# Kernel optimization log

Hardware: AMD Instinct MI355X
Metric: run time of the kernel (lower is better)

## Reference

```python
import jax, jax.numpy as jnp
import numpy as np

DIM = 1024
HEADS = 16
HEAD_DIM = DIM // HEADS
B, N = 2, 2048


def setup_inputs() -> dict:
    key = jax.random.key(0)
    k1, k2, k3, k4 = jax.random.split(key, 4)
    x = jax.random.normal(k1, (B, N, DIM), dtype=jnp.float32)
    # torch Linear weights: shape (out_features, in_features), y = x @ W.T + b
    w_qkv = jax.random.normal(k2, (3 * DIM, DIM), dtype=jnp.float32) * (DIM ** -0.5)
    w_proj = jax.random.normal(k3, (DIM, DIM), dtype=jnp.float32) * (DIM ** -0.5)
    b_proj = jax.random.normal(k4, (DIM,), dtype=jnp.float32) * 0.01
    return {"x": x, "w_qkv": w_qkv, "w_proj": w_proj, "b_proj": b_proj}


def reference(x, w_qkv, w_proj, b_proj):
    Bb, Nn, D = x.shape
    scale = HEAD_DIM ** -0.5
    qkv = x @ w_qkv.T                                # [B, N, 3D]
    qkv = qkv.reshape(Bb, Nn, 3, HEADS, HEAD_DIM)
    qkv = jnp.transpose(qkv, (2, 0, 3, 1, 4))        # [3, B, H, N, hd]
    q, k, v = qkv[0], qkv[1], qkv[2]
    attn = jnp.einsum('bhqd,bhkd->bhqk', q, k) * scale
    attn = jax.nn.softmax(attn, axis=-1)
    out = jnp.einsum('bhqk,bhkd->bhqd', attn, v)     # [B, H, N, hd]
    out = jnp.transpose(out, (0, 2, 1, 3)).reshape(Bb, Nn, D)
    return out @ w_proj.T + b_proj
```

## Files before the change

kernel.cpp:

```cpp
#include <hip/hip_runtime.h>
#include <cstdint>
#include <cstddef>

using u16 = unsigned short;
using u32 = uint32_t;
using f32x4  = __attribute__((ext_vector_type(4))) float;
using bf16x8 = __attribute__((ext_vector_type(8))) __bf16;
using s16x4  = __attribute__((ext_vector_type(4))) short;

#define D_MODEL 1024
#define N_HEADS 16
#define HD      64
#define SEQ     2048
#define QKV_LD  3072
#define K2SCALE 0.18033688011112042f

__device__ __forceinline__ u16 f2b(float f) {
  union { float f; u32 u; } v; v.f = f;
  u32 r = 0x7FFFu + ((v.u >> 16) & 1u);
  return (u16)((v.u + r) >> 16);
}

__device__ __forceinline__ u32 pkbf16(float a, float b) {
  return (u32)f2b(a) | ((u32)f2b(b) << 16);
}

#define MFMA16(A, B, C) __builtin_amdgcn_mfma_f32_16x16x16bf16_1k(A, B, C, 0, 0, 0)

__device__ __forceinline__ void gld16(const u16* g, u16* l) {
  __builtin_amdgcn_global_load_lds(
      (const __attribute__((address_space(1))) void*)g,
      (__attribute__((address_space(3))) void*)l, 16, 0, 0);
}

__global__ void cast_bf16(const float* __restrict__ src, u16* __restrict__ dst) {
  int i = blockIdx.x * blockDim.x + threadIdx.x;
  float4 f = ((const float4*)src)[i];
  ushort4 o;
  o.x = f2b(f.x); o.y = f2b(f.y); o.z = f2b(f.z); o.w = f2b(f.w);
  ((ushort4*)dst)[i] = o;
}

template<int OUTMODE>
__launch_bounds__(256, 2)
__global__ void gemm_nt(const u16* __restrict__ A, const u16* __restrict__ B,
                        u16* __restrict__ Ob, float* __restrict__ Of,
                        const float* __restrict__ bias, int N, int K) {
  __shared__ __attribute__((aligned(16))) u16 sA[128 * 32];
  __shared__ __attribute__((aligned(16))) u16 sB[128 * 32];

  const int tid  = threadIdx.x;
  const int lane = tid & 63;
  const int w    = tid >> 6;
  const int qd   = lane >> 4;
  const int ln   = lane & 15;
  const int wm   = (w >> 1) * 64;
  const int wn   = (w & 1) * 64;
  const int m0   = blockIdx.y * 128;
  const int n0   = blockIdx.x * 128;

  f32x4 acc[4][4] = {};

  for (int k0 = 0; k0 < K; k0 += 32) {
    __syncthreads();
    #pragma unroll
    for (int c = 0; c < 2; ++c) {
      int sbase = w * 128 + c * 64;
      int s = sbase + lane;
      int row = s >> 2, col = (s & 3) * 8;
      gld16(A + (size_t)(m0 + row) * K + k0 + col, &sA[sbase * 8]);
      gld16(B + (size_t)(n0 + row) * K + k0 + col, &sB[sbase * 8]);
    }
    __syncthreads();

    bf16x8 af[4], bfm[4];
    #pragma unroll
    for (int i = 0; i < 4; ++i) {
      af[i]  = *(const bf16x8*)&sA[(wm + i * 16 + ln) * 32 + qd * 8];
      bfm[i] = *(const bf16x8*)&sB[(wn + i * 16 + ln) * 32 + qd * 8];
    }
    #pragma unroll
    for (int i = 0; i < 4; ++i)
      #pragma unroll
      for (int j = 0; j < 4; ++j)
        acc[i][j] = __builtin_amdgcn_mfma_f32_16x16x32_bf16(af[i], bfm[j], acc[i][j], 0, 0, 0);
  }

  #pragma unroll
  for (int i = 0; i < 4; ++i) {
    #pragma unroll
    for (int j = 0; j < 4; ++j) {
      #pragma unroll
      for (int r = 0; r < 4; ++r) {
        int row = m0 + wm + i * 16 + qd * 4 + r;
        int col = n0 + wn + j * 16 + ln;
        float v = acc[i][j][r];
        if (OUTMODE == 0) {
          if (col < D_MODEL) v *= K2SCALE;
          Ob[(size_t)row * N + col] = f2b(v);
        } else {
          Of[(size_t)row * N + col] = v + bias[col];
        }
      }
    }
  }
}

__launch_bounds__(256, 4)
__global__ void attn_kernel(const u16* __restrict__ qkv, u16* __restrict__ outb) {
  __shared__ __attribute__((aligned(16))) u16 sK[2][128 * 32];
  __shared__ __attribute__((aligned(16))) u32 sVT[64 * 68];

  const int tid  = threadIdx.x;
  const int lane = tid & 63;
  const int w    = tid >> 6;
  const int qd   = lane >> 4;
  const int ln   = lane & 15;
  const int qt   = blockIdx.x;
  const int h    = blockIdx.y & 15;
  const int b    = blockIdx.y >> 4;
  const size_t tokbase = (size_t)b * SEQ;
  const int q0   = qt * 64;
  const int qoff = h * HD;
  const int koff = D_MODEL + h * HD;
  const int voff = 2 * D_MODEL + h * HD;

  bf16x8 aq[2];
  #pragma unroll
  for (int hf = 0; hf < 2; ++hf)
    aq[hf] = *(const bf16x8*)(qkv + (tokbase + q0 + w * 16 + ln) * QKV_LD
                              + qoff + hf * 32 + qd * 8);

  f32x4 accOT[4] = {};
  float psum = 0.0f;

  for (int kt = 0; kt < 16; ++kt) {
    const int kt0 = kt * 128;
    __syncthreads();
    #pragma unroll
    for (int hf = 0; hf < 2; ++hf) {
      #pragma unroll
      for (int c = 0; c < 2; ++c) {
        int sbase = w * 128 + c * 64;
        int s = sbase + lane;
        int row = s >> 2, col = (s & 3) * 8;
        gld16(qkv + (tokbase + kt0 + row) * QKV_LD + koff + hf * 32 + col,
              &sK[hf][sbase * 8]);
      }
    }
    #pragma unroll
    for (int it = 0; it < 2; ++it) {
      int j  = it * 256 + tid;
      int tp = j & 63;
      int d0 = (j >> 6) * 8;
      const u16* g0 = qkv + (tokbase + kt0 + tp * 2) * QKV_LD + voff + d0;
      union { uint4 q; u32 d[4]; } va, vb;
      va.q = *(const uint4*)g0;
      vb.q = *(const uint4*)(g0 + QKV_LD);
      #pragma unroll
      for (int e = 0; e < 4; ++e) {
        sVT[(d0 + 2 * e    ) * 68 + tp] = __builtin_amdgcn_perm(vb.d[e], va.d[e], 0x05040100u);
        sVT[(d0 + 2 * e + 1) * 68 + tp] = __builtin_amdgcn_perm(vb.d[e], va.d[e], 0x07060302u);
      }
    }
    __syncthreads();

    f32x4 accST[8] = {};
    #pragma unroll
    for (int cb = 0; cb < 8; ++cb) {
      #pragma unroll
      for (int hf = 0; hf < 2; ++hf) {
        bf16x8 ak = *(const bf16x8*)&sK[hf][(cb * 16 + ln) * 32 + qd * 8];
        accST[cb] = __builtin_amdgcn_mfma_f32_16x16x32_bf16(ak, aq[hf], accST[cb], 0, 0, 0);
      }
    }

    s16x4 pf[8];
    #pragma unroll
    for (int cb = 0; cb < 8; ++cb) {
      float p0 = __builtin_amdgcn_exp2f(accST[cb][0]);
      float p1 = __builtin_amdgcn_exp2f(accST[cb][1]);
      float p2 = __builtin_amdgcn_exp2f(accST[cb][2]);
      float p3 = __builtin_amdgcn_exp2f(accST[cb][3]);
      psum += (p0 + p1) + (p2 + p3);
      union { u32 d[2]; s16x4 v; } pk;
      pk.d[0] = pkbf16(p0, p1);
      pk.d[1] = pkbf16(p2, p3);
      pf[cb] = pk.v;
    }

    #pragma unroll
    for (int cb = 0; cb < 8; ++cb) {
      #pragma unroll
      for (int ob = 0; ob < 4; ++ob) {
        s16x4 vf = *(const s16x4*)&sVT[(ob * 16 + ln) * 68 + cb * 8 + qd * 2];
        accOT[ob] = MFMA16(vf, pf[cb], accOT[ob]);
      }
    }
  }

  psum += __shfl_xor(psum, 16, 64);
  psum += __shfl_xor(psum, 32, 64);
  const float rinv = 1.0f / psum;

  u16* sOut = (u16*)&sK[0][0];
  __syncthreads();
  #pragma unroll
  for (int ob = 0; ob < 4; ++ob) {
    u32 lo = pkbf16(accOT[ob][0] * rinv, accOT[ob][1] * rinv);
    u32 hi = pkbf16(accOT[ob][2] * rinv, accOT[ob][3] * rinv);
    ((u32*)sOut)[(w * 16 + ln) * 36 + ob * 8 + qd * 2    ] = lo;
    ((u32*)sOut)[(w * 16 + ln) * 36 + ob * 8 + qd * 2 + 1] = hi;
  }
  __syncthreads();
  #pragma unroll
  for (int it = 0; it < 2; ++it) {
    int idx = it * 256 + tid;
    int token = idx >> 3, chunk = idx & 7;
    uint4 v = *(const uint4*)&sOut[token * 72 + chunk * 8];
    *(uint4*)&outb[(tokbase + q0 + token) * D_MODEL + h * HD + chunk * 8] = v;
  }
}

extern "C" void kernel_launch(void* const* d_in, const int* in_sizes, int n_in,
                              void* d_out, int out_size, void* d_ws, size_t ws_size,
                              hipStream_t stream) {
  const float* x      = (const float*)d_in[0];
  const float* w_qkv  = (const float*)d_in[1];
  const float* w_proj = (const float*)d_in[2];
  const float* b_proj = (const float*)d_in[3];
  float* out = (float*)d_out;

  u16* ws     = (u16*)d_ws;
  u16* xb     = ws;
  u16* wqkvb  = xb    + (size_t)4096 * 1024;
  u16* wprojb = wqkvb + (size_t)3072 * 1024;
  u16* qkvb   = wprojb + (size_t)1024 * 1024;
  u16* attnb  = qkvb  + (size_t)4096 * 3072;

  cast_bf16<<<4096, 256, 0, stream>>>(x,      xb);
  cast_bf16<<<3072, 256, 0, stream>>>(w_qkv,  wqkvb);
  cast_bf16<<<1024, 256, 0, stream>>>(w_proj, wprojb);

  gemm_nt<0><<<dim3(24, 32), 256, 0, stream>>>(xb, wqkvb, qkvb, nullptr, nullptr, 3072, 1024);

  attn_kernel<<<dim3(32, 32), 256, 0, stream>>>(qkvb, attnb);

  gemm_nt<1><<<dim3(8, 32), 256, 0, stream>>>(attnb, wprojb, nullptr, out, b_proj, 1024, 1024);
}
```

Measured before the change: 224.1 us.

## Double-buffer attention K/V tiles, process 128 queries per block, shrink proj GEMM tile

The attention kernel now double-buffers K and transposed V in shared memory. It prefetches the next tile's V into registers one iteration ahead and handles two 64-query groups per block, so each K/V tile is reused twice and load latency overlaps compute. Scores are computed and consumed per 16-key chunk instead of being kept for the full 128-key tile. The GEMM gains an M-tile template parameter, and the output projection uses 64-row tiles to launch more blocks, with launch bounds changed to 3 waves per SIMD. In exchange, shared memory and registers per block rise, attention occupancy drops to 2 blocks, and the attention grid halves to 512 blocks.

```diff
diff --git a/kernel.cpp b/kernel.cpp
--- a/kernel.cpp
+++ b/kernel.cpp
@@ -41,12 +41,12 @@
   ((ushort4*)dst)[i] = o;
 }
 
-template<int OUTMODE>
-__launch_bounds__(256, 2)
+template<int OUTMODE, int MT>
+__launch_bounds__(256, 3)
 __global__ void gemm_nt(const u16* __restrict__ A, const u16* __restrict__ B,
                         u16* __restrict__ Ob, float* __restrict__ Of,
                         const float* __restrict__ bias, int N, int K) {
-  __shared__ __attribute__((aligned(16))) u16 sA[128 * 32];
+  __shared__ __attribute__((aligned(16))) u16 sA[MT * 32];
   __shared__ __attribute__((aligned(16))) u16 sB[128 * 32];
 
   const int tid  = threadIdx.x;
@@ -54,40 +54,48 @@
   const int w    = tid >> 6;
   const int qd   = lane >> 4;
   const int ln   = lane & 15;
-  const int wm   = (w >> 1) * 64;
+  constexpr int MI = MT / 32;
+  const int wm   = (w >> 1) * (MT / 2);
   const int wn   = (w & 1) * 64;
-  const int m0   = blockIdx.y * 128;
+  const int m0   = blockIdx.y * MT;
   const int n0   = blockIdx.x * 128;
 
-  f32x4 acc[4][4] = {};
+  f32x4 acc[MI][4] = {};
 
   for (int k0 = 0; k0 < K; k0 += 32) {
     __syncthreads();
+    #pragma unroll
+    for (int c = 0; c < MT / 64; ++c) {
+      int sbase = w * MT + c * 64;
+      int s = sbase + lane;
+      int row = s >> 2, col = (s & 3) * 8;
+      gld16(A + (size_t)(m0 + row) * K + k0 + col, &sA[sbase * 8]);
+    }
     #pragma unroll
     for (int c = 0; c < 2; ++c) {
       int sbase = w * 128 + c * 64;
       int s = sbase + lane;
       int row = s >> 2, col = (s & 3) * 8;
-      gld16(A + (size_t)(m0 + row) * K + k0 + col, &sA[sbase * 8]);
       gld16(B + (size_t)(n0 + row) * K + k0 + col, &sB[sbase * 8]);
     }
     __syncthreads();
 
-    bf16x8 af[4], bfm[4];
-    #pragma unroll
-    for (int i = 0; i < 4; ++i) {
-      af[i]  = *(const bf16x8*)&sA[(wm + i * 16 + ln) * 32 + qd * 8];
-      bfm[i] = *(const bf16x8*)&sB[(wn + i * 16 + ln) * 32 + qd * 8];
-    }
-    #pragma unroll
-    for (int i = 0; i < 4; ++i)
+    bf16x8 af[MI], bfm[4];
+    #pragma unroll
+    for (int i = 0; i < MI; ++i)
+      af[i] = *(const bf16x8*)&sA[(wm + i * 16 + ln) * 32 + qd * 8];
+    #pragma unroll
+    for (int j = 0; j < 4; ++j)
+      bfm[j] = *(const bf16x8*)&sB[(wn + j * 16 + ln) * 32 + qd * 8];
+    #pragma unroll
+    for (int i = 0; i < MI; ++i)
       #pragma unroll
       for (int j = 0; j < 4; ++j)
         acc[i][j] = __builtin_amdgcn_mfma_f32_16x16x32_bf16(af[i], bfm[j], acc[i][j], 0, 0, 0);
   }
 
   #pragma unroll
-  for (int i = 0; i < 4; ++i) {
+  for (int i = 0; i < MI; ++i) {
     #pragma unroll
     for (int j = 0; j < 4; ++j) {
       #pragma unroll
@@ -106,115 +114,140 @@
   }
 }
 
-__launch_bounds__(256, 4)
+__launch_bounds__(256, 2)
 __global__ void attn_kernel(const u16* __restrict__ qkv, u16* __restrict__ outb) {
-  __shared__ __attribute__((aligned(16))) u16 sK[2][128 * 32];
-  __shared__ __attribute__((aligned(16))) u32 sVT[64 * 68];
+  __shared__ __attribute__((aligned(16))) u16 sK[2][2][128 * 32];
+  __shared__ __attribute__((aligned(16))) u32 sVT[2][64 * 68];
 
   const int tid  = threadIdx.x;
   const int lane = tid & 63;
   const int w    = tid >> 6;
   const int qd   = lane >> 4;
   const int ln   = lane & 15;
-  const int qt   = blockIdx.x;
+  const int qp   = blockIdx.x;
   const int h    = blockIdx.y & 15;
   const int b    = blockIdx.y >> 4;
   const size_t tokbase = (size_t)b * SEQ;
-  const int q0   = qt * 64;
+  const int q0   = qp * 128;
   const int qoff = h * HD;
   const int koff = D_MODEL + h * HD;
   const int voff = 2 * D_MODEL + h * HD;
 
-  bf16x8 aq[2];
-  #pragma unroll
-  for (int hf = 0; hf < 2; ++hf)
-    aq[hf] = *(const bf16x8*)(qkv + (tokbase + q0 + w * 16 + ln) * QKV_LD
-                              + qoff + hf * 32 + qd * 8);
-
-  f32x4 accOT[4] = {};
-  float psum = 0.0f;
-
-  for (int kt = 0; kt < 16; ++kt) {
-    const int kt0 = kt * 128;
-    __syncthreads();
-    #pragma unroll
-    for (int hf = 0; hf < 2; ++hf) {
+  bf16x8 aq[2][2];
+  #pragma unroll
+  for (int c2 = 0; c2 < 2; ++c2)
+    #pragma unroll
+    for (int hf = 0; hf < 2; ++hf)
+      aq[c2][hf] = *(const bf16x8*)(qkv + (tokbase + q0 + c2 * 64 + w * 16 + ln) * QKV_LD
+                                    + qoff + hf * 32 + qd * 8);
+
+  auto stageK = [&](int kt, int buf) {
+    #pragma unroll
+    for (int hf = 0; hf < 2; ++hf)
       #pragma unroll
       for (int c = 0; c < 2; ++c) {
         int sbase = w * 128 + c * 64;
         int s = sbase + lane;
         int row = s >> 2, col = (s & 3) * 8;
-        gld16(qkv + (tokbase + kt0 + row) * QKV_LD + koff + hf * 32 + col,
-              &sK[hf][sbase * 8]);
-      }
-    }
+        gld16(qkv + (tokbase + kt * 128 + row) * QKV_LD + koff + hf * 32 + col,
+              &sK[buf][hf][sbase * 8]);
+      }
+  };
+  auto loadV = [&](int kt, uint4* va, uint4* vb) {
     #pragma unroll
     for (int it = 0; it < 2; ++it) {
-      int j  = it * 256 + tid;
-      int tp = j & 63;
-      int d0 = (j >> 6) * 8;
-      const u16* g0 = qkv + (tokbase + kt0 + tp * 2) * QKV_LD + voff + d0;
-      union { uint4 q; u32 d[4]; } va, vb;
-      va.q = *(const uint4*)g0;
-      vb.q = *(const uint4*)(g0 + QKV_LD);
+      int j = it * 256 + tid;
+      int tp = j & 63, d0 = (j >> 6) * 8;
+      const u16* g0 = qkv + (tokbase + kt * 128 + tp * 2) * QKV_LD + voff + d0;
+      va[it] = *(const uint4*)g0;
+      vb[it] = *(const uint4*)(g0 + QKV_LD);
+    }
+  };
+  auto writeV = [&](int buf, const uint4* va, const uint4* vb) {
+    #pragma unroll
+    for (int it = 0; it < 2; ++it) {
+      int j = it * 256 + tid;
+      int tp = j & 63, d0 = (j >> 6) * 8;
+      const u32* a  = (const u32*)&va[it];
+      const u32* bb = (const u32*)&vb[it];
       #pragma unroll
       for (int e = 0; e < 4; ++e) {
-        sVT[(d0 + 2 * e    ) * 68 + tp] = __builtin_amdgcn_perm(vb.d[e], va.d[e], 0x05040100u);
-        sVT[(d0 + 2 * e + 1) * 68 + tp] = __builtin_amdgcn_perm(vb.d[e], va.d[e], 0x07060302u);
-      }
-    }
+        sVT[buf][(d0 + 2 * e    ) * 68 + tp] = __builtin_amdgcn_perm(bb[e], a[e], 0x05040100u);
+        sVT[buf][(d0 + 2 * e + 1) * 68 + tp] = __builtin_amdgcn_perm(bb[e], a[e], 0x07060302u);
+      }
+    }
+  };
+
+  stageK(0, 0);
+  uint4 va[2], vb[2];
+  loadV(0, va, vb);
+  writeV(0, va, vb);
+  loadV(1, va, vb);
+
+  f32x4 accOT[2][4] = {};
+  float psum[2] = {0.f, 0.f};
+
+  for (int kt = 0; kt < 16; ++kt) {
+    const int cur = kt & 1, nxt = cur ^ 1;
     __syncthreads();
-
-    f32x4 accST[8] = {};
+    if (kt < 15) { stageK(kt + 1, nxt); writeV(nxt, va, vb); }
+    if (kt < 14) { loadV(kt + 2, va, vb); }
+
     #pragma unroll
     for (int cb = 0; cb < 8; ++cb) {
-      #pragma unroll
-      for (int hf = 0; hf < 2; ++hf) {
-        bf16x8 ak = *(const bf16x8*)&sK[hf][(cb * 16 + ln) * 32 + qd * 8];
-        accST[cb] = __builtin_amdgcn_mfma_f32_16x16x32_bf16(ak, aq[hf], accST[cb], 0, 0, 0);
-      }
-    }
-
-    s16x4 pf[8];
-    #pragma unroll
-    for (int cb = 0; cb < 8; ++cb) {
-      float p0 = __builtin_amdgcn_exp2f(accST[cb][0]);
-      float p1 = __builtin_amdgcn_exp2f(accST[cb][1]);
-      float p2 = __builtin_amdgcn_exp2f(accST[cb][2]);
-      float p3 = __builtin_amdgcn_exp2f(accST[cb][3]);
-      psum += (p0 + p1) + (p2 + p3);
-      union { u32 d[2]; s16x4 v; } pk;
-      pk.d[0] = pkbf16(p0, p1);
-      pk.d[1] = pkbf16(p2, p3);
-      pf[cb] = pk.v;
-    }
-
-    #pragma unroll
-    for (int cb = 0; cb < 8; ++cb) {
+      bf16x8 ak0 = *(const bf16x8*)&sK[cur][0][(cb * 16 + ln) * 32 + qd * 8];
+      bf16x8 ak1 = *(const bf16x8*)&sK[cur][1][(cb * 16 + ln) * 32 + qd * 8];
+      f32x4 st[2];
+      #pragma unroll
+      for (int c2 = 0; c2 < 2; ++c2) {
+        f32x4 z = {0.f, 0.f, 0.f, 0.f};
+        f32x4 t = __builtin_amdgcn_mfma_f32_16x16x32_bf16(ak0, aq[c2][0], z, 0, 0, 0);
+        st[c2]  = __builtin_amdgcn_mfma_f32_16x16x32_bf16(ak1, aq[c2][1], t, 0, 0, 0);
+      }
+      s16x4 pf[2];
+      #pragma unroll
+      for (int c2 = 0; c2 < 2; ++c2) {
+        float p0 = __builtin_amdgcn_exp2f(st[c2][0]);
+        float p1 = __builtin_amdgcn_exp2f(st[c2][1]);
+        float p2 = __builtin_amdgcn_exp2f(st[c2][2]);
+        float p3 = __builtin_amdgcn_exp2f(st[c2][3]);
+        psum[c2] += (p0 + p1) + (p2 + p3);
+        union { u32 d[2]; s16x4 v; } pk;
+        pk.d[0] = pkbf16(p0, p1);
+        pk.d[1] = pkbf16(p2, p3);
+        pf[c2] = pk.v;
+      }
       #pragma unroll
       for (int ob = 0; ob < 4; ++ob) {
-        s16x4 vf = *(const s16x4*)&sVT[(ob * 16 + ln) * 68 + cb * 8 + qd * 2];
-        accOT[ob] = MFMA16(vf, pf[cb], accOT[ob]);
-      }
-    }
-  }
-
-  psum += __shfl_xor(psum, 16, 64);
-  psum += __shfl_xor(psum, 32, 64);
-  const float rinv = 1.0f / psum;
-
-  u16* sOut = (u16*)&sK[0][0];
+        s16x4 vf = *(const s16x4*)&sVT[cur][(ob * 16 + ln) * 68 + cb * 8 + qd * 2];
+        accOT[0][ob] = MFMA16(vf, pf[0], accOT[0][ob]);
+        accOT[1][ob] = MFMA16(vf, pf[1], accOT[1][ob]);
+      }
+    }
+  }
+
+  #pragma unroll
+  for (int c2 = 0; c2 < 2; ++c2) {
+    float s = psum[c2];
+    s += __shfl_xor(s, 16, 64);
+    s += __shfl_xor(s, 32, 64);
+    psum[c2] = 1.0f / s;
+  }
+
+  u16* sOut = (u16*)&sK[0][0][0];
   __syncthreads();
   #pragma unroll
-  for (int ob = 0; ob < 4; ++ob) {
-    u32 lo = pkbf16(accOT[ob][0] * rinv, accOT[ob][1] * rinv);
-    u32 hi = pkbf16(accOT[ob][2] * rinv, accOT[ob][3] * rinv);
-    ((u32*)sOut)[(w * 16 + ln) * 36 + ob * 8 + qd * 2    ] = lo;
-    ((u32*)sOut)[(w * 16 + ln) * 36 + ob * 8 + qd * 2 + 1] = hi;
-  }
+  for (int c2 = 0; c2 < 2; ++c2)
+    #pragma unroll
+    for (int ob = 0; ob < 4; ++ob) {
+      u32 lo = pkbf16(accOT[c2][ob][0] * psum[c2], accOT[c2][ob][1] * psum[c2]);
+      u32 hi = pkbf16(accOT[c2][ob][2] * psum[c2], accOT[c2][ob][3] * psum[c2]);
+      ((u32*)sOut)[(c2 * 64 + w * 16 + ln) * 36 + ob * 8 + qd * 2    ] = lo;
+      ((u32*)sOut)[(c2 * 64 + w * 16 + ln) * 36 + ob * 8 + qd * 2 + 1] = hi;
+    }
   __syncthreads();
   #pragma unroll
-  for (int it = 0; it < 2; ++it) {
+  for (int it = 0; it < 4; ++it) {
     int idx = it * 256 + tid;
     int token = idx >> 3, chunk = idx & 7;
     uint4 v = *(const uint4*)&sOut[token * 72 + chunk * 8];
@@ -242,9 +275,9 @@
   cast_bf16<<<3072, 256, 0, stream>>>(w_qkv,  wqkvb);
   cast_bf16<<<1024, 256, 0, stream>>>(w_proj, wprojb);
 
-  gemm_nt<0><<<dim3(24, 32), 256, 0, stream>>>(xb, wqkvb, qkvb, nullptr, nullptr, 3072, 1024);
-
-  attn_kernel<<<dim3(32, 32), 256, 0, stream>>>(qkvb, attnb);
-
-  gemm_nt<1><<<dim3(8, 32), 256, 0, stream>>>(attnb, wprojb, nullptr, out, b_proj, 1024, 1024);
-}
+  gemm_nt<0, 128><<<dim3(24, 32), 256, 0, stream>>>(xb, wqkvb, qkvb, nullptr, nullptr, 3072, 1024);
+
+  attn_kernel<<<dim3(16, 32), 256, 0, stream>>>(qkvb, attnb);
+
+  gemm_nt<1, 64><<<dim3(8, 64), 256, 0, stream>>>(attnb, wprojb, nullptr, out, b_proj, 1024, 1024);
+}
```

After: 200.3 us. 10.6% less time.
